# Optimization experiments

Hardware: AMD Instinct MI355X
Metric: run time of the kernel (lower is better)

Reference implementation:

```python
import jax, jax.numpy as jnp
import numpy as np

B, S, H = 1, 2048, 2048
NH, NKV, HD = 16, 4, 128
F, E, TOPK = 4096, 8, 2
EPS = 1e-5
THETA = 10000.0
NEG = -1e30


def setup_inputs() -> dict:
    key = jax.random.key(0)
    ks = jax.random.split(key, 12)
    s = 0.02
    f32 = jnp.float32
    return {
        "positions": jnp.arange(S, dtype=jnp.int32),
        "hidden_states": jax.random.normal(ks[0], (B, S, H), f32),
        "wq": jax.random.normal(ks[1], (H, NH * HD), f32) * s,
        "wk": jax.random.normal(ks[2], (H, NKV * HD), f32) * s,
        "wv": jax.random.normal(ks[3], (H, NKV * HD), f32) * s,
        "wo": jax.random.normal(ks[4], (NH * HD, H), f32) * s,
        "w_gate": jax.random.normal(ks[5], (H, E), f32) * s,
        "w1": jax.random.normal(ks[6], (E, H, F), f32) * s,
        "w2": jax.random.normal(ks[7], (E, F, H), f32) * s,
        "w3": jax.random.normal(ks[8], (E, H, F), f32) * s,
        "ln_in": jnp.ones((H,), f32),
        "ln_post": jnp.ones((H,), f32),
    }


def rmsnorm(x, w):
    var = jnp.mean(jnp.square(x.astype(jnp.float32)), axis=-1, keepdims=True)
    return (x.astype(jnp.float32) * jax.lax.rsqrt(var + EPS)).astype(x.dtype) * w


def apply_rope(x, positions):
    # x: [B, S, n, HD], neox style (rotate halves)
    half = HD // 2
    inv_freq = 1.0 / (THETA ** (jnp.arange(half, dtype=jnp.float32) * 2.0 / HD))
    ang = positions.astype(jnp.float32)[:, None] * inv_freq  # [S, half]
    cos = jnp.cos(ang)[None, :, None, :]
    sin = jnp.sin(ang)[None, :, None, :]
    x1, x2 = jnp.split(x, 2, axis=-1)
    return jnp.concatenate([x1 * cos - x2 * sin, x2 * cos + x1 * sin], axis=-1).astype(x.dtype)


def decoder_layer(positions, x, wq, wk, wv, wo, w_gate, w1, w2, w3, ln_in, ln_post):
    # residual is None branch: residual = x; h = input_layernorm(x)
    residual = x
    h = rmsnorm(x, ln_in)
    # --- attention ---
    q = (h @ wq).reshape(B, S, NH, HD)
    k = (h @ wk).reshape(B, S, NKV, HD)
    v = (h @ wv).reshape(B, S, NKV, HD)
    q = apply_rope(q, positions)
    k = apply_rope(k, positions)
    rep = NH // NKV  # GQA: repeat kv heads
    k = jnp.repeat(k, rep, axis=2)
    v = jnp.repeat(v, rep, axis=2)
    scores = jnp.einsum("bqhd,bkhd->bhqk", q, k) * (HD ** -0.5)
    causal = jnp.tril(jnp.ones((S, S), bool))
    scores = jnp.where(causal[None, None], scores, NEG)
    attn = jax.nn.softmax(scores, axis=-1)
    o = jnp.einsum("bhqk,bkhd->bqhd", attn, v).reshape(B, S, NH * HD) @ wo
    # --- fused add + post-attention RMSNorm ---
    residual = o + residual
    h = rmsnorm(residual, ln_post)
    # --- MoE: dense all-expert compute, mask-weighted combine ---
    xt = h.reshape(-1, H)  # [T, H]
    logits = xt @ w_gate
    rw = jax.nn.softmax(logits.astype(jnp.float32), axis=-1)  # [T, E]
    w_top, idx = jax.lax.top_k(rw, TOPK)
    w_top = w_top / jnp.sum(w_top, axis=-1, keepdims=True)
    T = xt.shape[0]
    combine = jnp.zeros((T, E), jnp.float32).at[jnp.arange(T)[:, None], idx].add(w_top)
    a = jnp.einsum("th,ehf->etf", xt, w1)  # [E, T, F]
    g = jax.nn.silu(a) * jnp.einsum("th,ehf->etf", xt, w3)
    out = jnp.einsum("etf,efh->eth", g, w2)  # [E, T, H]
    moe = jnp.einsum("eth,te->th", out, combine.astype(xt.dtype))
    return moe.reshape(B, S, H), residual


def reference(positions, hidden_states, wq, wk, wv, wo, w_gate, w1, w2, w3, ln_in, ln_post):
    return decoder_layer(positions, hidden_states, wq, wk, wv, wo, w_gate, w1, w2, w3, ln_in, ln_post)
```

## Files before the change

kernel.cpp:

```cpp
#include <hip/hip_runtime.h>

typedef _Float16 f16x8 __attribute__((ext_vector_type(8)));
typedef _Float16 f16x2 __attribute__((ext_vector_type(2)));
typedef float f32x4 __attribute__((ext_vector_type(4)));

#define DEV __device__ __forceinline__

struct alignas(16) H8 { _Float16 h[8]; };
struct alignas(8)  H4 { _Float16 h[4]; };

union U8 { f16x2 v[4]; f16x8 x; H8 h; };
union U4 { f16x2 v[2]; H4 h; unsigned int u[2]; };

DEV f32x4 mfma16(f16x8 a, f16x8 b, f32x4 c) {
  return __builtin_amdgcn_mfma_f32_16x16x32_f16(a, b, c, 0, 0, 0);
}

DEV f16x2 pkrtz(float a, float b) {
  return __builtin_bit_cast(f16x2, __builtin_amdgcn_cvt_pkrtz(a, b));
}

DEV void split8v(const float* t, f16x8& hi, f16x8& lo) {
  U8 H_, L_;
  #pragma unroll
  for (int j = 0; j < 4; ++j) {
    f16x2 hh = pkrtz(t[2*j], t[2*j+1]);
    float r0 = t[2*j]   - (float)hh[0];
    float r1 = t[2*j+1] - (float)hh[1];
    H_.v[j] = hh;
    L_.v[j] = pkrtz(r0, r1);
  }
  hi = H_.x; lo = L_.x;
}

DEV void packpair(float a, float b, f16x2& hi, f16x2& lo) {
  f16x2 hh = pkrtz(a, b);
  lo = pkrtz(a - (float)hh[0], b - (float)hh[1]);
  hi = hh;
}

DEV f16x8 frag_b36(const _Float16* b, int n, int kc) {
  const unsigned long long* p = (const unsigned long long*)(b + n*36 + kc*8);
  union { unsigned long long u[2]; f16x8 v; } r;
  r.u[0] = p[0]; r.u[1] = p[1];
  return r.v;
}

DEV float block_sum(float v, volatile float* red, int tid) {
  #pragma unroll
  for (int mm = 1; mm < 64; mm <<= 1) v += __shfl_xor(v, mm);
  if ((tid & 63) == 0) red[tid >> 6] = v;
  __syncthreads();
  return red[0] + red[1] + red[2] + red[3];
}

__global__ __launch_bounds__(256) void k_rmsnorm_split(
    const float* __restrict__ x, const float* __restrict__ w,
    _Float16* __restrict__ hi, _Float16* __restrict__ lo) {
  __shared__ float red[4];
  int row = blockIdx.x, tid = threadIdx.x;
  const float* xr = x + (size_t)row*2048 + tid*8;
  float xs[8];
  *(float4*)&xs[0] = *(const float4*)xr;
  *(float4*)&xs[4] = *(const float4*)(xr + 4);
  float ss = 0.f;
  #pragma unroll
  for (int j = 0; j < 8; ++j) ss += xs[j]*xs[j];
  float tot = block_sum(ss, red, tid);
  float sc = 1.0f / sqrtf(tot*(1.0f/2048.0f) + 1e-5f);
  const float* wr = w + tid*8;
  H8 ph, pl;
  #pragma unroll
  for (int j = 0; j < 8; ++j) {
    float o = xs[j]*sc*wr[j];
    _Float16 hh = (_Float16)o;
    ph.h[j] = hh; pl.h[j] = (_Float16)(o - (float)hh);
  }
  *(H8*)(hi + (size_t)row*2048 + tid*8) = ph;
  *(H8*)(lo + (size_t)row*2048 + tid*8) = pl;
}

__global__ __launch_bounds__(256) void k_gemm_ks(
    const _Float16* __restrict__ Ahi, const _Float16* __restrict__ Alo,
    const float* __restrict__ B, int N, int K,
    float* __restrict__ C) {
  const int tid = threadIdx.x;
  const int l = tid & 63, w = tid >> 6;
  const int wm = w >> 1, wn = w & 1;
  const int row0 = blockIdx.y * 128, col0 = blockIdx.x * 128;
  const int kz = K / gridDim.z;
  const int kbase = blockIdx.z * kz;

  __shared__ _Float16 aHi[128*32], aLo[128*32];
  __shared__ _Float16 bHi[128*36], bLo[128*36];

  f32x4 acc[4][4] = {};

  const int rS = tid >> 1, khalf = tid & 1;
  const int cg = tid & 31, rg = tid >> 5;

  for (int k0 = kbase; k0 < kbase + kz; k0 += 32) {
    __syncthreads();
    {
      int c0 = khalf*2;
      int d0 = rS*32 + ((c0    ) ^ (rS&3))*8;
      int d1 = rS*32 + ((c0 + 1) ^ (rS&3))*8;
      const _Float16* ah = Ahi + (size_t)(row0 + rS)*K + k0 + khalf*16;
      const _Float16* al = Alo + (size_t)(row0 + rS)*K + k0 + khalf*16;
      *(H8*)&aHi[d0] = *(const H8*)ah;
      *(H8*)&aHi[d1] = *(const H8*)(ah + 8);
      *(H8*)&aLo[d0] = *(const H8*)al;
      *(H8*)&aLo[d1] = *(const H8*)(al + 8);
    }
    {
      const float* bp = B + (size_t)(k0 + rg*4)*N + col0 + cg*4;
      float4 v0 = *(const float4*)bp;
      float4 v1 = *(const float4*)(bp + N);
      float4 v2 = *(const float4*)(bp + 2*(size_t)N);
      float4 v3 = *(const float4*)(bp + 3*(size_t)N);
      const float* r0 = (const float*)&v0;
      const float* r1 = (const float*)&v1;
      const float* r2 = (const float*)&v2;
      const float* r3 = (const float*)&v3;
      #pragma unroll
      for (int j = 0; j < 4; ++j) {
        U4 hu, lu;
        packpair(r0[j], r1[j], hu.v[0], lu.v[0]);
        packpair(r2[j], r3[j], hu.v[1], lu.v[1]);
        int ei = (cg*4 + j)*36 + rg*4;
        *(H4*)&bHi[ei] = hu.h;
        *(H4*)&bLo[ei] = lu.h;
      }
    }
    __syncthreads();
    {
      const int kc = l >> 4;
      f16x8 ah[4], al4[4];
      #pragma unroll
      for (int m = 0; m < 4; ++m) {
        int mr = wm*64 + m*16 + (l & 15);
        int cc = (kc ^ (mr & 3))*8;
        ah[m]  = *(const f16x8*)&aHi[mr*32 + cc];
        al4[m] = *(const f16x8*)&aLo[mr*32 + cc];
      }
      #pragma unroll
      for (int n = 0; n < 4; ++n) {
        int nr = wn*64 + n*16 + (l & 15);
        f16x8 bh = frag_b36(bHi, nr, kc);
        f16x8 bl = frag_b36(bLo, nr, kc);
        #pragma unroll
        for (int m = 0; m < 4; ++m) {
          acc[m][n] = mfma16(ah[m],  bh, acc[m][n]);
          acc[m][n] = mfma16(ah[m],  bl, acc[m][n]);
          acc[m][n] = mfma16(al4[m], bh, acc[m][n]);
        }
      }
    }
  }
  #pragma unroll
  for (int m = 0; m < 4; ++m)
    #pragma unroll
    for (int n = 0; n < 4; ++n)
      #pragma unroll
      for (int r = 0; r < 4; ++r) {
        int row = row0 + wm*64 + m*16 + (l>>4)*4 + r;
        int col = col0 + wn*64 + n*16 + (l&15);
        atomicAdd(&C[(size_t)row*N + col], acc[m][n][r]);
      }
}

__global__ __launch_bounds__(256) void k_rope(
    float* __restrict__ buf, const int* __restrict__ pos, int nh) {
  int s = blockIdx.x;
  int hh = blockIdx.y*4 + (threadIdx.x >> 6);
  int d = threadIdx.x & 63;
  float p = (float)pos[s];
  double ex = ((double)(2*d)/128.0) * 9.210340371976184;
  float pw = (float)exp(ex);
  float inv = 1.0f / pw;
  float ang = p * inv;
  float cs = cosf(ang), sn = sinf(ang);
  float* b = buf + (size_t)s*(nh*128) + hh*128 + d;
  float x1 = b[0], x2 = b[64];
  b[0]  = x1*cs - x2*sn;
  b[64] = x2*cs + x1*sn;
}

__global__ __launch_bounds__(256) void k_attn(
    const float* __restrict__ q, const float* __restrict__ k,
    const float* __restrict__ v,
    _Float16* __restrict__ o_hi, _Float16* __restrict__ o_lo) {
  const int qt = gridDim.x - 1 - blockIdx.x;
  const int h = blockIdx.y;
  const int tid = threadIdx.x, l = tid & 63, w = tid >> 6;
  const int qb = qt*64, qw = qb + w*16;
  const int kvh = h >> 2;

  __shared__ _Float16 kHi[32*128], kLo[32*128];
  __shared__ _Float16 vHi[128*32], vLo[128*32];
  __shared__ _Float16 pHi[4][16*40], pLo[4][16*40];

  f16x8 qh[4], ql[4];
  {
    int qrow = qw + (l & 15);
    const float* qp = q + (size_t)qrow*2048 + h*128 + (l>>4)*8;
    #pragma unroll
    for (int c = 0; c < 4; ++c) {
      float t[8];
      *(float4*)&t[0] = *(const float4*)(qp + c*32);
      *(float4*)&t[4] = *(const float4*)(qp + c*32 + 4);
      split8v(t, qh[c], ql[c]);
    }
  }

  float mrun[4], lrun[4];
  f32x4 oacc[8] = {};
  #pragma unroll
  for (int r = 0; r < 4; ++r) { mrun[r] = -1e30f; lrun[r] = 0.f; }

  const int srow = tid >> 3, sc = (tid & 7)*2;

  for (int kv0 = 0; kv0 <= qb + 32; kv0 += 32) {
    __syncthreads();
    {
      const float* kp = k + (size_t)(kv0 + srow)*512 + kvh*128 + sc*8;
      const float* vp = v + (size_t)(kv0 + srow)*512 + kvh*128 + sc*8;
      #pragma unroll
      for (int cc = 0; cc < 2; ++cc) {
        int c = sc + cc;
        float tk[8];
        *(float4*)&tk[0] = *(const float4*)(kp + cc*8);
        *(float4*)&tk[4] = *(const float4*)(kp + cc*8 + 4);
        f16x8 hx, lx;
        split8v(tk, hx, lx);
        int di = srow*128 + (c ^ (srow & 7))*8;
        *(H8*)&kHi[di] = *(const H8*)&hx;
        *(H8*)&kLo[di] = *(const H8*)&lx;
        float tv_[8];
        *(float4*)&tv_[0] = *(const float4*)(vp + cc*8);
        *(float4*)&tv_[4] = *(const float4*)(vp + cc*8 + 4);
        #pragma unroll
        for (int j = 0; j < 8; ++j) {
          float x = tv_[j];
          _Float16 hh = (_Float16)x;
          _Float16 ll = (_Float16)(x - (float)hh);
          int d = c*8 + j;
          int vi = d*32 + (((srow>>3) ^ (d&3)))*8 + (srow & 7);
          vHi[vi] = hh; vLo[vi] = ll;
        }
      }
    }
    __syncthreads();
    if (kv0 <= qw + 15) {
      f32x4 s[2] = {};
      #pragma unroll
      for (int nt = 0; nt < 2; ++nt) {
        int krow = nt*16 + (l & 15);
        #pragma unroll
        for (int c = 0; c < 4; ++c) {
          int ch = (c*4 + (l>>4)) ^ (krow & 7);
          f16x8 bh = *(const f16x8*)&kHi[krow*128 + ch*8];
          f16x8 bl = *(const f16x8*)&kLo[krow*128 + ch*8];
          s[nt] = mfma16(qh[c], bh, s[nt]);
          s[nt] = mfma16(qh[c], bl, s[nt]);
          s[nt] = mfma16(ql[c], bh, s[nt]);
        }
      }
      const float SC = 0.08838834764831845f;
      float sv[2][4];
      #pragma unroll
      for (int nt = 0; nt < 2; ++nt)
        #pragma unroll
        for (int r = 0; r < 4; ++r) {
          float val = s[nt][r]*SC;
          int qg = qw + (l>>4)*4 + r;
          int kg = kv0 + nt*16 + (l & 15);
          sv[nt][r] = (kg > qg) ? -1e30f : val;
        }
      float tm[4];
      #pragma unroll
      for (int r = 0; r < 4; ++r) tm[r] = fmaxf(sv[0][r], sv[1][r]);
      #pragma unroll
      for (int mm = 1; mm < 16; mm <<= 1)
        #pragma unroll
        for (int r = 0; r < 4; ++r) tm[r] = fmaxf(tm[r], __shfl_xor(tm[r], mm));
      float alpha[4], rs[4];
      #pragma unroll
      for (int r = 0; r < 4; ++r) {
        float mn = fmaxf(mrun[r], tm[r]);
        alpha[r] = expf(mrun[r] - mn);
        mrun[r] = mn;
      }
      float pv[2][4];
      #pragma unroll
      for (int nt = 0; nt < 2; ++nt)
        #pragma unroll
        for (int r = 0; r < 4; ++r) pv[nt][r] = expf(sv[nt][r] - mrun[r]);
      #pragma unroll
      for (int r = 0; r < 4; ++r) rs[r] = pv[0][r] + pv[1][r];
      #pragma unroll
      for (int mm = 1; mm < 16; mm <<= 1)
        #pragma unroll
        for (int r = 0; r < 4; ++r) rs[r] += __shfl_xor(rs[r], mm);
      #pragma unroll
      for (int r = 0; r < 4; ++r) lrun[r] = lrun[r]*alpha[r] + rs[r];
      #pragma unroll
      for (int dt = 0; dt < 8; ++dt)
        #pragma unroll
        for (int r = 0; r < 4; ++r) oacc[dt][r] *= alpha[r];
      #pragma unroll
      for (int nt = 0; nt < 2; ++nt)
        #pragma unroll
        for (int r = 0; r < 4; ++r) {
          float x = pv[nt][r];
          _Float16 hh = (_Float16)x;
          int qr = (l>>4)*4 + r, kc = nt*16 + (l & 15);
          pHi[w][qr*40 + kc] = hh;
          pLo[w][qr*40 + kc] = (_Float16)(x - (float)hh);
        }
      f16x8 pa = *(const f16x8*)&pHi[w][(l&15)*40 + (l>>4)*8];
      f16x8 pb = *(const f16x8*)&pLo[w][(l&15)*40 + (l>>4)*8];
      #pragma unroll
      for (int dt = 0; dt < 8; ++dt) {
        int d = dt*16 + (l & 15);
        int ch = ((l>>4) ^ (d & 3))*8;
        f16x8 vh = *(const f16x8*)&vHi[d*32 + ch];
        f16x8 vl = *(const f16x8*)&vLo[d*32 + ch];
        oacc[dt] = mfma16(pa, vh, oacc[dt]);
        oacc[dt] = mfma16(pa, vl, oacc[dt]);
        oacc[dt] = mfma16(pb, vh, oacc[dt]);
      }
    }
  }
  #pragma unroll
  for (int dt = 0; dt < 8; ++dt)
    #pragma unroll
    for (int r = 0; r < 4; ++r) {
      int qg = qw + (l>>4)*4 + r;
      float ov = oacc[dt][r] / lrun[r];
      _Float16 hh = (_Float16)ov;
      size_t idx = (size_t)qg*2048 + h*128 + dt*16 + (l&15);
      o_hi[idx] = hh;
      o_lo[idx] = (_Float16)(ov - (float)hh);
    }
}

__global__ __launch_bounds__(256) void k_postnorm_gate(
    const float* __restrict__ resid, const float* __restrict__ wln,
    const float* __restrict__ wg, _Float16* __restrict__ h2,
    float* __restrict__ logits) {
  __shared__ float red[4];
  __shared__ float red2[4][8];
  int row = blockIdx.x, tid = threadIdx.x;
  const float* xr = resid + (size_t)row*2048 + tid*8;
  float xs[8];
  *(float4*)&xs[0] = *(const float4*)xr;
  *(float4*)&xs[4] = *(const float4*)(xr + 4);
  float ss = 0.f;
  #pragma unroll
  for (int j = 0; j < 8; ++j) ss += xs[j]*xs[j];
  float tot = block_sum(ss, red, tid);
  float sc = 1.0f/sqrtf(tot*(1.0f/2048.0f) + 1e-5f);
  const float* wr = wln + tid*8;
  float hv[8];
  H8 ph;
  #pragma unroll
  for (int j = 0; j < 8; ++j) {
    hv[j] = xs[j]*sc*wr[j];
    ph.h[j] = (_Float16)hv[j];
  }
  *(H8*)(h2 + (size_t)row*2048 + tid*8) = ph;
  float lg[8] = {0,0,0,0,0,0,0,0};
  const float* wgp = wg + (size_t)tid*8*8;
  #pragma unroll
  for (int j = 0; j < 8; ++j)
    #pragma unroll
    for (int e = 0; e < 8; ++e) lg[e] += hv[j]*wgp[j*8 + e];
  #pragma unroll
  for (int mm = 1; mm < 64; mm <<= 1)
    #pragma unroll
    for (int e = 0; e < 8; ++e) lg[e] += __shfl_xor(lg[e], mm);
  if ((tid & 63) == 0)
    #pragma unroll
    for (int e = 0; e < 8; ++e) red2[tid>>6][e] = lg[e];
  __syncthreads();
  if (tid < 8)
    logits[(size_t)row*8 + tid] = red2[0][tid]+red2[1][tid]+red2[2][tid]+red2[3][tid];
}

__global__ __launch_bounds__(256) void k_route(
    const float* __restrict__ logits, int* __restrict__ counts,
    int* __restrict__ slot_tok, float* __restrict__ slot_w) {
  int t = blockIdx.x*256 + threadIdx.x;
  if (t >= 2048) return;
  float lg[8];
  #pragma unroll
  for (int e = 0; e < 8; ++e) lg[e] = logits[t*8 + e];
  int a = 0; float la = lg[0];
  #pragma unroll
  for (int e = 1; e < 8; ++e) if (lg[e] > la) { la = lg[e]; a = e; }
  int b = -1; float lb = -3e38f;
  #pragma unroll
  for (int e = 0; e < 8; ++e) if (e != a && lg[e] > lb) { lb = lg[e]; b = e; }
  float wa = 1.f/(1.f + expf(lb - la));
  float wb = 1.f - wa;
  int sa = atomicAdd(&counts[a], 1);
  slot_tok[a*2048 + sa] = t; slot_w[a*2048 + sa] = wa;
  int sb = atomicAdd(&counts[b], 1);
  slot_tok[b*2048 + sb] = t; slot_w[b*2048 + sb] = wb;
}

__global__ void k_scan(const int* __restrict__ counts, int* __restrict__ offs) {
  if (threadIdx.x == 0) {
    int o_ = 0;
    #pragma unroll
    for (int e = 0; e < 8; ++e) { offs[e] = o_; o_ += counts[e]; }
  }
}

__global__ __launch_bounds__(256) void k_moe1(
    const _Float16* __restrict__ h2, const float* __restrict__ w1,
    const float* __restrict__ w3, const int* __restrict__ counts,
    const int* __restrict__ offs, const int* __restrict__ slot_tok,
    _Float16* __restrict__ g) {
  int bid = blockIdx.x;
  int e = bid >> 10, mt = (bid >> 6) & 15, nt = bid & 63;
  int cnt = counts[e];
  if (mt*128 >= cnt) return;
  const int tid = threadIdx.x, l = tid & 63, w = tid >> 6;
  const int wm = w >> 1, wn = w & 1;
  __shared__ _Float16 aT[128*32];
  __shared__ _Float16 b1[64*36], b3[64*36];
  const int rS = tid >> 1, khalf = tid & 1;
  int slot = mt*128 + rS;
  int tok = (slot < cnt) ? slot_tok[e*2048 + slot] : slot_tok[e*2048];
  const _Float16* arow = h2 + (size_t)tok*2048;
  const int cg = tid & 15, rg = tid >> 4;
  const float* w1p = w1 + (size_t)e*2048*4096 + nt*64 + cg*4 + (size_t)rg*2*4096;
  const float* w3p = w3 + (size_t)e*2048*4096 + nt*64 + cg*4 + (size_t)rg*2*4096;
  f32x4 acc1[4][2] = {}, acc3[4][2] = {};
  for (int k0 = 0; k0 < 2048; k0 += 32) {
    __syncthreads();
    {
      const _Float16* ap = arow + k0 + khalf*16;
      int c0 = khalf*2;
      *(H8*)&aT[rS*32 + ((c0  )^(rS&3))*8] = *(const H8*)ap;
      *(H8*)&aT[rS*32 + ((c0+1)^(rS&3))*8] = *(const H8*)(ap + 8);
    }
    {
      const float* p1 = w1p + (size_t)k0*4096;
      float4 a0 = *(const float4*)p1;
      float4 a1 = *(const float4*)(p1 + 4096);
      const float* p3 = w3p + (size_t)k0*4096;
      float4 c0_ = *(const float4*)p3;
      float4 c1 = *(const float4*)(p3 + 4096);
      const float* x0 = (const float*)&a0;
      const float* x1 = (const float*)&a1;
      const float* y0 = (const float*)&c0_;
      const float* y1 = (const float*)&c1;
      #pragma unroll
      for (int j = 0; j < 4; ++j) {
        int ei = (cg*4 + j)*36 + rg*2;
        *(f16x2*)&b1[ei] = pkrtz(x0[j], x1[j]);
        *(f16x2*)&b3[ei] = pkrtz(y0[j], y1[j]);
      }
    }
    __syncthreads();
    {
      const int kc = l >> 4;
      f16x8 a_[4];
      #pragma unroll
      for (int m = 0; m < 4; ++m) {
        int mr = wm*64 + m*16 + (l & 15);
        a_[m] = *(const f16x8*)&aT[mr*32 + (kc ^ (mr&3))*8];
      }
      #pragma unroll
      for (int n = 0; n < 2; ++n) {
        int nr = wn*32 + n*16 + (l & 15);
        f16x8 bb1 = frag_b36(b1, nr, kc);
        f16x8 bb3 = frag_b36(b3, nr, kc);
        #pragma unroll
        for (int m = 0; m < 4; ++m) {
          acc1[m][n] = mfma16(a_[m], bb1, acc1[m][n]);
          acc3[m][n] = mfma16(a_[m], bb3, acc3[m][n]);
        }
      }
    }
  }
  int ge = offs[e];
  #pragma unroll
  for (int m = 0; m < 4; ++m)
    #pragma unroll
    for (int n = 0; n < 2; ++n)
      #pragma unroll
      for (int r = 0; r < 4; ++r) {
        int srow2 = mt*128 + wm*64 + m*16 + (l>>4)*4 + r;
        if (srow2 < cnt) {
          float x1 = acc1[m][n][r], x3 = acc3[m][n][r];
          float gg = (x1/(1.f + expf(-x1)))*x3;
          int col = nt*64 + wn*32 + n*16 + (l&15);
          g[(size_t)(ge + srow2)*4096 + col] = (_Float16)gg;
        }
      }
}

__global__ __launch_bounds__(256) void k_moe2(
    const _Float16* __restrict__ g, const float* __restrict__ w2,
    const int* __restrict__ counts, const int* __restrict__ offs,
    const int* __restrict__ slot_tok, const float* __restrict__ slot_w,
    float* __restrict__ out) {
  int bid = blockIdx.x;
  int e = bid >> 8, mt = (bid >> 4) & 15, nt = bid & 15;
  int cnt = counts[e];
  if (mt*128 >= cnt) return;
  const int tid = threadIdx.x, l = tid & 63, w = tid >> 6;
  const int wm = w >> 1, wn = w & 1;
  __shared__ _Float16 aT[128*32];
  __shared__ _Float16 bT[128*36];
  const int rS = tid >> 1, khalf = tid & 1;
  int ge = offs[e];
  int slot = mt*128 + rS;
  const _Float16* arow = g + (size_t)(ge + (slot < cnt ? slot : 0))*4096;
  const int cg = tid & 31, rg = tid >> 5;
  const float* w2p = w2 + (size_t)e*4096*2048 + nt*128 + cg*4 + (size_t)rg*4*2048;
  f32x4 acc[4][4] = {};
  for (int k0 = 0; k0 < 4096; k0 += 32) {
    __syncthreads();
    {
      const _Float16* ap = arow + k0 + khalf*16;
      int c0 = khalf*2;
      *(H8*)&aT[rS*32 + ((c0  )^(rS&3))*8] = *(const H8*)ap;
      *(H8*)&aT[rS*32 + ((c0+1)^(rS&3))*8] = *(const H8*)(ap + 8);
    }
    {
      const float* p = w2p + (size_t)k0*2048;
      float4 v0 = *(const float4*)p;
      float4 v1 = *(const float4*)(p + 2048);
      float4 v2 = *(const float4*)(p + 2*(size_t)2048);
      float4 v3 = *(const float4*)(p + 3*(size_t)2048);
      const float* r0 = (const float*)&v0;
      const float* r1 = (const float*)&v1;
      const float* r2 = (const float*)&v2;
      const float* r3 = (const float*)&v3;
      #pragma unroll
      for (int j = 0; j < 4; ++j) {
        U4 u;
        u.v[0] = pkrtz(r0[j], r1[j]);
        u.v[1] = pkrtz(r2[j], r3[j]);
        *(H4*)&bT[(cg*4 + j)*36 + rg*4] = u.h;
      }
    }
    __syncthreads();
    {
      const int kc = l >> 4;
      f16x8 a_[4];
      #pragma unroll
      for (int m = 0; m < 4; ++m) {
        int mr = wm*64 + m*16 + (l&15);
        a_[m] = *(const f16x8*)&aT[mr*32 + (kc ^ (mr&3))*8];
      }
      #pragma unroll
      for (int n = 0; n < 4; ++n) {
        f16x8 bb = frag_b36(bT, wn*64 + n*16 + (l&15), kc);
        #pragma unroll
        for (int m = 0; m < 4; ++m) acc[m][n] = mfma16(a_[m], bb, acc[m][n]);
      }
    }
  }
  #pragma unroll
  for (int m = 0; m < 4; ++m)
    #pragma unroll
    for (int r = 0; r < 4; ++r) {
      int srow2 = mt*128 + wm*64 + m*16 + (l>>4)*4 + r;
      if (srow2 < cnt) {
        int tok = slot_tok[e*2048 + srow2];
        float wt = slot_w[e*2048 + srow2];
        #pragma unroll
        for (int n = 0; n < 4; ++n) {
          int col = nt*128 + wn*64 + n*16 + (l&15);
          atomicAdd(&out[(size_t)tok*2048 + col], wt*acc[m][n][r]);
        }
      }
    }
}

extern "C" void kernel_launch(void* const* d_in, const int* in_sizes, int n_in,
                              void* d_out, int out_size, void* d_ws, size_t ws_size,
                              hipStream_t stream) {
  const int*   positions = (const int*)d_in[0];
  const float* x   = (const float*)d_in[1];
  const float* wq  = (const float*)d_in[2];
  const float* wk  = (const float*)d_in[3];
  const float* wv  = (const float*)d_in[4];
  const float* wo  = (const float*)d_in[5];
  const float* wg  = (const float*)d_in[6];
  const float* w1  = (const float*)d_in[7];
  const float* w2  = (const float*)d_in[8];
  const float* w3  = (const float*)d_in[9];
  const float* ln_in   = (const float*)d_in[10];
  const float* ln_post = (const float*)d_in[11];

  float* moe_out   = (float*)d_out;
  float* resid_out = (float*)d_out + (size_t)4194304;

  char* ws = (char*)d_ws;
  _Float16* h_hi   = (_Float16*)(ws);
  _Float16* h_lo   = (_Float16*)(ws + 8388608);
  float*    qbuf   = (float*)(ws + 16777216);
  float*    kbuf   = (float*)(ws + 33554432);
  float*    vbuf   = (float*)(ws + 37748736);
  _Float16* o_hi   = (_Float16*)(ws + 41943040);
  _Float16* o_lo   = (_Float16*)(ws + 50331648);
  _Float16* h2     = (_Float16*)(ws + 58720256);
  float*    logits = (float*)(ws + 67108864);
  int*      counts = (int*)(ws + 67174400);
  int*      offs   = (int*)(ws + 67174656);
  int*      slot_tok = (int*)(ws + 67174912);
  float*    slot_w   = (float*)(ws + 67240448);
  _Float16* gbuf   = (_Float16*)ws;

  hipMemsetAsync(qbuf, 0, 16777216, stream);
  hipMemsetAsync(kbuf, 0, 4194304, stream);
  hipMemsetAsync(vbuf, 0, 4194304, stream);
  hipMemcpyAsync(resid_out, x, (size_t)4194304*4, hipMemcpyDeviceToDevice, stream);
  hipMemsetAsync(moe_out, 0, (size_t)4194304*4, stream);
  hipMemsetAsync(counts, 0, 32, stream);

  k_rmsnorm_split<<<2048, 256, 0, stream>>>(x, ln_in, h_hi, h_lo);
  k_gemm_ks<<<dim3(16,16,2), 256, 0, stream>>>(h_hi, h_lo, wq, 2048, 2048, qbuf);
  k_gemm_ks<<<dim3(4,16,4),  256, 0, stream>>>(h_hi, h_lo, wk,  512, 2048, kbuf);
  k_gemm_ks<<<dim3(4,16,4),  256, 0, stream>>>(h_hi, h_lo, wv,  512, 2048, vbuf);
  k_rope<<<dim3(2048,4), 256, 0, stream>>>(qbuf, positions, 16);
  k_rope<<<dim3(2048,1), 256, 0, stream>>>(kbuf, positions, 4);
  k_attn<<<dim3(32,16), 256, 0, stream>>>(qbuf, kbuf, vbuf, o_hi, o_lo);
  k_gemm_ks<<<dim3(16,16,2), 256, 0, stream>>>(o_hi, o_lo, wo, 2048, 2048, resid_out);
  k_postnorm_gate<<<2048, 256, 0, stream>>>(resid_out, ln_post, wg, h2, logits);
  k_route<<<8, 256, 0, stream>>>(logits, counts, slot_tok, slot_w);
  k_scan<<<1, 64, 0, stream>>>(counts, offs);
  k_moe1<<<8192, 256, 0, stream>>>(h2, w1, w3, counts, offs, slot_tok, gbuf);
  k_moe2<<<2048, 256, 0, stream>>>(gbuf, w2, counts, offs, slot_tok, slot_w, moe_out);
}
```

Baseline: 1.127 ms.

## Register-prefetch MoE GEMM tiles and add split-K to moe2 and q/o projections

Both MoE GEMM kernels now load the next K-slice from global memory into registers while the current slice is computed, then write it to LDS at the top of the next iteration. This hides global load latency behind the MFMA work. moe2 also becomes split-K over two halves of F via blockIdx.y, doubling its grid. The q and o projection GEMMs go from split-K 2 to 4. The split-K changes depend on the output being accumulated atomically, which the zero-initialised or pre-copied output buffers suggest, and they add more atomic traffic in exchange for more parallel blocks.

After: 1.541 ms. +36.7%, slower.

```diff
diff --git a/kernel.cpp b/kernel.cpp
--- a/kernel.cpp
+++ b/kernel.cpp
@@ -439,33 +439,42 @@
   const float* w1p = w1 + (size_t)e*2048*4096 + nt*64 + cg*4 + (size_t)rg*2*4096;
   const float* w3p = w3 + (size_t)e*2048*4096 + nt*64 + cg*4 + (size_t)rg*2*4096;
   f32x4 acc1[4][2] = {}, acc3[4][2] = {};
-  for (int k0 = 0; k0 < 2048; k0 += 32) {
-    __syncthreads();
-    {
-      const _Float16* ap = arow + k0 + khalf*16;
-      int c0 = khalf*2;
-      *(H8*)&aT[rS*32 + ((c0  )^(rS&3))*8] = *(const H8*)ap;
-      *(H8*)&aT[rS*32 + ((c0+1)^(rS&3))*8] = *(const H8*)(ap + 8);
-    }
-    {
-      const float* p1 = w1p + (size_t)k0*4096;
-      float4 a0 = *(const float4*)p1;
-      float4 a1 = *(const float4*)(p1 + 4096);
-      const float* p3 = w3p + (size_t)k0*4096;
-      float4 c0_ = *(const float4*)p3;
-      float4 c1 = *(const float4*)(p3 + 4096);
-      const float* x0 = (const float*)&a0;
-      const float* x1 = (const float*)&a1;
-      const float* y0 = (const float*)&c0_;
-      const float* y1 = (const float*)&c1;
-      #pragma unroll
-      for (int j = 0; j < 4; ++j) {
-        int ei = (cg*4 + j)*36 + rg*2;
-        *(f16x2*)&b1[ei] = pkrtz(x0[j], x1[j]);
-        *(f16x2*)&b3[ei] = pkrtz(y0[j], y1[j]);
-      }
-    }
-    __syncthreads();
+  H8 ta0, ta1;
+  float4 tb10, tb11, tb30, tb31;
+
+  auto LOAD = [&](int k0) {
+    const _Float16* ap = arow + k0 + khalf*16;
+    ta0 = *(const H8*)ap;
+    ta1 = *(const H8*)(ap + 8);
+    const float* p1 = w1p + (size_t)k0*4096;
+    tb10 = *(const float4*)p1;
+    tb11 = *(const float4*)(p1 + 4096);
+    const float* p3 = w3p + (size_t)k0*4096;
+    tb30 = *(const float4*)p3;
+    tb31 = *(const float4*)(p3 + 4096);
+  };
+  auto WRITE = [&]() {
+    int c0 = khalf*2;
+    *(H8*)&aT[rS*32 + ((c0  )^(rS&3))*8] = ta0;
+    *(H8*)&aT[rS*32 + ((c0+1)^(rS&3))*8] = ta1;
+    const float* x0 = (const float*)&tb10;
+    const float* x1 = (const float*)&tb11;
+    const float* y0 = (const float*)&tb30;
+    const float* y1 = (const float*)&tb31;
+    #pragma unroll
+    for (int j = 0; j < 4; ++j) {
+      int ei = (cg*4 + j)*36 + rg*2;
+      *(f16x2*)&b1[ei] = pkrtz(x0[j], x1[j]);
+      *(f16x2*)&b3[ei] = pkrtz(y0[j], y1[j]);
+    }
+  };
+
+  LOAD(0);
+  for (int kk = 0; kk < 64; ++kk) {
+    __syncthreads();
+    WRITE();
+    __syncthreads();
+    if (kk < 63) LOAD((kk+1)*32);
     {
       const int kc = l >> 4;
       f16x8 a_[4];
@@ -523,34 +532,44 @@
   const _Float16* arow = g + (size_t)(ge + (slot < cnt ? slot : 0))*4096;
   const int cg = tid & 31, rg = tid >> 5;
   const float* w2p = w2 + (size_t)e*4096*2048 + nt*128 + cg*4 + (size_t)rg*4*2048;
+  const int kbase = blockIdx.y * 2048;
   f32x4 acc[4][4] = {};
-  for (int k0 = 0; k0 < 4096; k0 += 32) {
-    __syncthreads();
-    {
-      const _Float16* ap = arow + k0 + khalf*16;
-      int c0 = khalf*2;
-      *(H8*)&aT[rS*32 + ((c0  )^(rS&3))*8] = *(const H8*)ap;
-      *(H8*)&aT[rS*32 + ((c0+1)^(rS&3))*8] = *(const H8*)(ap + 8);
-    }
-    {
-      const float* p = w2p + (size_t)k0*2048;
-      float4 v0 = *(const float4*)p;
-      float4 v1 = *(const float4*)(p + 2048);
-      float4 v2 = *(const float4*)(p + 2*(size_t)2048);
-      float4 v3 = *(const float4*)(p + 3*(size_t)2048);
-      const float* r0 = (const float*)&v0;
-      const float* r1 = (const float*)&v1;
-      const float* r2 = (const float*)&v2;
-      const float* r3 = (const float*)&v3;
-      #pragma unroll
-      for (int j = 0; j < 4; ++j) {
-        U4 u;
-        u.v[0] = pkrtz(r0[j], r1[j]);
-        u.v[1] = pkrtz(r2[j], r3[j]);
-        *(H4*)&bT[(cg*4 + j)*36 + rg*4] = u.h;
-      }
-    }
-    __syncthreads();
+  H8 ta0, ta1;
+  float4 tb0, tb1, tb2, tb3;
+
+  auto LOAD = [&](int k0) {
+    const _Float16* ap = arow + k0 + khalf*16;
+    ta0 = *(const H8*)ap;
+    ta1 = *(const H8*)(ap + 8);
+    const float* p = w2p + (size_t)k0*2048;
+    tb0 = *(const float4*)p;
+    tb1 = *(const float4*)(p + 2048);
+    tb2 = *(const float4*)(p + 2*(size_t)2048);
+    tb3 = *(const float4*)(p + 3*(size_t)2048);
+  };
+  auto WRITE = [&]() {
+    int c0 = khalf*2;
+    *(H8*)&aT[rS*32 + ((c0  )^(rS&3))*8] = ta0;
+    *(H8*)&aT[rS*32 + ((c0+1)^(rS&3))*8] = ta1;
+    const float* r0 = (const float*)&tb0;
+    const float* r1 = (const float*)&tb1;
+    const float* r2 = (const float*)&tb2;
+    const float* r3 = (const float*)&tb3;
+    #pragma unroll
+    for (int j = 0; j < 4; ++j) {
+      U4 u;
+      u.v[0] = pkrtz(r0[j], r1[j]);
+      u.v[1] = pkrtz(r2[j], r3[j]);
+      *(H4*)&bT[(cg*4 + j)*36 + rg*4] = u.h;
+    }
+  };
+
+  LOAD(kbase);
+  for (int kk = 0; kk < 64; ++kk) {
+    __syncthreads();
+    WRITE();
+    __syncthreads();
+    if (kk < 63) LOAD(kbase + (kk+1)*32);
     {
       const int kc = l >> 4;
       f16x8 a_[4];
@@ -627,16 +646,16 @@
   hipMemsetAsync(counts, 0, 32, stream);
 
   k_rmsnorm_split<<<2048, 256, 0, stream>>>(x, ln_in, h_hi, h_lo);
-  k_gemm_ks<<<dim3(16,16,2), 256, 0, stream>>>(h_hi, h_lo, wq, 2048, 2048, qbuf);
+  k_gemm_ks<<<dim3(16,16,4), 256, 0, stream>>>(h_hi, h_lo, wq, 2048, 2048, qbuf);
   k_gemm_ks<<<dim3(4,16,4),  256, 0, stream>>>(h_hi, h_lo, wk,  512, 2048, kbuf);
   k_gemm_ks<<<dim3(4,16,4),  256, 0, stream>>>(h_hi, h_lo, wv,  512, 2048, vbuf);
   k_rope<<<dim3(2048,4), 256, 0, stream>>>(qbuf, positions, 16);
   k_rope<<<dim3(2048,1), 256, 0, stream>>>(kbuf, positions, 4);
   k_attn<<<dim3(32,16), 256, 0, stream>>>(qbuf, kbuf, vbuf, o_hi, o_lo);
-  k_gemm_ks<<<dim3(16,16,2), 256, 0, stream>>>(o_hi, o_lo, wo, 2048, 2048, resid_out);
+  k_gemm_ks<<<dim3(16,16,4), 256, 0, stream>>>(o_hi, o_lo, wo, 2048, 2048, resid_out);
   k_postnorm_gate<<<2048, 256, 0, stream>>>(resid_out, ln_post, wg, h2, logits);
   k_route<<<8, 256, 0, stream>>>(logits, counts, slot_tok, slot_w);
   k_scan<<<1, 64, 0, stream>>>(counts, offs);
   k_moe1<<<8192, 256, 0, stream>>>(h2, w1, w3, counts, offs, slot_tok, gbuf);
-  k_moe2<<<2048, 256, 0, stream>>>(gbuf, w2, counts, offs, slot_tok, slot_w, moe_out);
-}
+  k_moe2<<<dim3(2048,2), 256, 0, stream>>>(gbuf, w2, counts, offs, slot_tok, slot_w, moe_out);
+}
```
